# Optimization experiments

Measured on AMD Instinct MI355X. Metric: run time of the kernel, lower is better.

The kernel has to match this reference:

```python
import jax, jax.numpy as jnp
import numpy as np

B, T, C = 4, 1024, 2048
H, DN, DR = 16, 128, 64
D = DN + DR  # 192
Q_RANK, KV_RANK = 1536, 512
ROPE_BASE = 10000.0


def rope_cos_sin(seq_len, dim, dtype=jnp.float32):
    inv_freq = 1.0 / (ROPE_BASE ** (jnp.arange(0, dim, 2, dtype=jnp.float32) / dim))
    t = jnp.arange(seq_len, dtype=jnp.float32)
    freqs = jnp.outer(t, inv_freq)  # [T, dim/2]
    return jnp.cos(freqs).astype(dtype), jnp.sin(freqs).astype(dtype)


def apply_rope(x, cos, sin):
    # x: [B, T, H, Dr], cos/sin: [T, Dr/2]; interleaved-pair rotation (Llama style)
    x1 = x[..., 0::2]
    x2 = x[..., 1::2]
    c = cos[None, :, None, :]
    s = sin[None, :, None, :]
    o1 = x1 * c - x2 * s
    o2 = x1 * s + x2 * c
    return jnp.stack([o1, o2], axis=-1).reshape(x.shape)


def setup_inputs() -> dict:
    key = jax.random.key(0)
    ks = jax.random.split(key, 9)
    def g(k, shape, scale):
        return jax.random.normal(k, shape, dtype=jnp.float32) * scale
    return {
        "x": g(ks[0], (B, T, C), 1.0),
        "wq_down": g(ks[1], (C, Q_RANK), C ** -0.5),
        "wq_nope": g(ks[2], (Q_RANK, H * DN), Q_RANK ** -0.5),
        "wq_rope": g(ks[3], (Q_RANK, H * DR), Q_RANK ** -0.5),
        "wkv_down": g(ks[4], (C, KV_RANK), C ** -0.5),
        "wv_up": g(ks[5], (KV_RANK, H * D), KV_RANK ** -0.5),
        "wk_nope": g(ks[6], (KV_RANK, H * DN), KV_RANK ** -0.5),
        "wk_rope": g(ks[7], (KV_RANK, H * DR), KV_RANK ** -0.5),
        "wo": g(ks[8], (H * D, C), (H * D) ** -0.5),
    }


def reference(x, wq_down, wq_nope, wq_rope, wkv_down, wv_up, wk_nope, wk_rope, wo):
    b, t, c = x.shape
    q_latent = x @ wq_down            # [B,T,Q_RANK]
    kv_latent = x @ wkv_down          # [B,T,KV_RANK]
    q_c = (q_latent @ wq_nope).reshape(b, t, H, DN)
    q_r = (q_latent @ wq_rope).reshape(b, t, H, DR)
    v = (kv_latent @ wv_up).reshape(b, t, H, D)
    k_c = (kv_latent @ wk_nope).reshape(b, t, H, DN)
    k_r = (kv_latent @ wk_rope).reshape(b, t, H, DR)

    cos, sin = rope_cos_sin(t, DR, x.dtype)
    q_r = apply_rope(q_r, cos, sin)
    k_r = apply_rope(k_r, cos, sin)

    q = jnp.concatenate([q_c, q_r], axis=-1)  # [B,T,H,D]
    k = jnp.concatenate([k_c, k_r], axis=-1)  # [B,T,H,D]

    scale = 1.0 / (D ** 0.5)
    scores = jnp.einsum("bthd,bshd->bhts", q, k) * scale  # [B,H,T,T]
    causal = jnp.tril(jnp.ones((t, t), dtype=bool))
    scores = jnp.where(causal[None, None], scores, jnp.finfo(scores.dtype).min)
    probs = jax.nn.softmax(scores, axis=-1)
    out = jnp.einsum("bhts,bshd->bthd", probs, v).reshape(b, t, H * D)
    return out @ wo
```

## Files before the change

kernel.cpp:

```cpp
#include <hip/hip_runtime.h>

typedef unsigned short u16;
typedef __bf16  bf16x8 __attribute__((ext_vector_type(8)));
typedef short   short8 __attribute__((ext_vector_type(8)));
typedef float   f32x4  __attribute__((ext_vector_type(4)));
typedef u16     u16x4  __attribute__((ext_vector_type(4)));

__device__ __forceinline__ u16 f2bf(float f) {
  unsigned b = __builtin_bit_cast(unsigned, f);
  b += 0x7fffu + ((b >> 16) & 1u);
  return (u16)(b >> 16);
}
__device__ __forceinline__ float bf2f(u16 u) {
  return __builtin_bit_cast(float, (unsigned)u << 16);
}
__device__ __forceinline__ f32x4 mfma16(short8 a, short8 b, f32x4 c) {
  return __builtin_amdgcn_mfma_f32_16x16x32_bf16(
      __builtin_bit_cast(bf16x8, a), __builtin_bit_cast(bf16x8, b), c, 0, 0, 0);
}
__device__ __forceinline__ void gload_lds16(const void* g, void* l) {
  __builtin_amdgcn_global_load_lds(
      (const __attribute__((address_space(1))) void*)g,
      (__attribute__((address_space(3))) void*)l, 16, 0, 0);
}

#define VMCNT(n) asm volatile("s_waitcnt vmcnt(" #n ")" ::: "memory")
#define LGKMCNT(n) asm volatile("s_waitcnt lgkmcnt(" #n ")" ::: "memory")
#define MEMFENCE asm volatile("" ::: "memory")

__global__ __launch_bounds__(256) void castk(const float* __restrict__ in,
                                             u16* __restrict__ out, int n4) {
  int i = blockIdx.x * 256 + threadIdx.x;
  if (i >= n4) return;
  float4 v = ((const float4*)in)[i];
  u16x4 o;
  o[0] = f2bf(v.x); o[1] = f2bf(v.y); o[2] = f2bf(v.z); o[3] = f2bf(v.w);
  *(u16x4*)&out[i * 4] = o;
}

__global__ __launch_bounds__(256) void wcast(
    const float* __restrict__ wqd, const float* __restrict__ wqn,
    const float* __restrict__ wqr, const float* __restrict__ wkd,
    const float* __restrict__ wvu, const float* __restrict__ wkn,
    const float* __restrict__ wkr, const float* __restrict__ wo,
    u16* __restrict__ W1t, u16* __restrict__ Wqt,
    u16* __restrict__ Wkvt, u16* __restrict__ Wot) {
  __shared__ float tile[64][65];
  const int bid = blockIdx.x;
  const float* W; u16* Wt; int K, N, lid;
  if (bid < 768)       { W = wqd; Wt = W1t;                 K = 2048; N = 1536; lid = bid; }
  else if (bid < 1024) { W = wkd; Wt = W1t + 1536ull * 2048; K = 2048; N = 512;  lid = bid - 768; }
  else if (bid < 1792) { W = wqn; Wt = Wqt;                 K = 1536; N = 2048; lid = bid - 1024; }
  else if (bid < 2176) { W = wqr; Wt = Wqt + 2048ull * 1536; K = 1536; N = 1024; lid = bid - 1792; }
  else if (bid < 2432) { W = wkn; Wt = Wkvt;                K = 512;  N = 2048; lid = bid - 2176; }
  else if (bid < 2560) { W = wkr; Wt = Wkvt + 2048ull * 512; K = 512;  N = 1024; lid = bid - 2432; }
  else if (bid < 2944) { W = wvu; Wt = Wkvt + 3072ull * 512; K = 512;  N = 3072; lid = bid - 2560; }
  else                 { W = wo;  Wt = Wot;                 K = 3072; N = 2048; lid = bid - 2944; }
  const int kb = K >> 6;
  const int k0 = (lid % kb) * 64, n0 = (lid / kb) * 64;
  const int tid = threadIdx.x;
  const int lane4 = (tid & 15) * 4, grp = tid >> 4;
#pragma unroll
  for (int p = 0; p < 4; ++p) {
    int r = p * 16 + grp;
    float4 v = *(const float4*)&W[(size_t)(k0 + r) * N + n0 + lane4];
    tile[r][lane4]     = v.x;
    tile[r][lane4 + 1] = v.y;
    tile[r][lane4 + 2] = v.z;
    tile[r][lane4 + 3] = v.w;
  }
  __syncthreads();
  const int n = tid >> 2, ks = (tid & 3) * 16;
  short8 s0, s1;
#pragma unroll
  for (int j = 0; j < 8; ++j) s0[j] = (short)f2bf(tile[ks + j][n]);
#pragma unroll
  for (int j = 0; j < 8; ++j) s1[j] = (short)f2bf(tile[ks + 8 + j][n]);
  u16* dst = Wt + (size_t)(n0 + n) * K + k0 + ks;
  *(short8*)dst = s0;
  *(short8*)(dst + 8) = s1;
}

template <int EPI>
__global__ __launch_bounds__(512, 2) void gemm_p8(const u16* __restrict__ A, int lda,
                                                  const u16* __restrict__ Bt, int ldb,
                                                  void* __restrict__ out0,
                                                  void* __restrict__ out1,
                                                  void* __restrict__ out2, int ldc,
                                                  int K) {
  __shared__ char smem[147456];
  const int tid = threadIdx.x;
  const int w = tid >> 6, l = tid & 63;
  const int wr = w >> 2, wc = w & 3;
  const int lr = l & 15, hi = l >> 4, lg4 = hi * 4;

  const int nbx = gridDim.x;
  int id = blockIdx.y * nbx + blockIdx.x;
  int cpx = (nbx * gridDim.y) >> 3;
  int sid = (id & 7) * cpx + (id >> 3);
  const int m0 = (sid % nbx) * 128, n0 = (sid / nbx) * 256;

  const u16* asrc[2];
  const u16* bsrc[4];
#pragma unroll
  for (int j = 0; j < 2; ++j) {
    int lin = j * 8192 + tid * 16;
    int row = lin >> 7, colb = lin & 127;
    asrc[j] = A + (size_t)(m0 + row) * lda + ((colb ^ ((row & 7) << 4)) >> 1);
  }
#pragma unroll
  for (int j = 0; j < 4; ++j) {
    int lin = j * 8192 + tid * 16;
    int row = lin >> 7, colb = lin & 127;
    bsrc[j] = Bt + (size_t)(n0 + row) * ldb + ((colb ^ ((row & 7) << 4)) >> 1);
  }

  int aoff[4], boff[4];
#pragma unroll
  for (int m = 0; m < 4; ++m) {
    int row = wr * 64 + m * 16 + lr;
    aoff[m] = row * 128 + ((hi * 16) ^ ((row & 7) << 4));
  }
#pragma unroll
  for (int n = 0; n < 4; ++n) {
    int row = wc * 64 + n * 16 + lr;
    boff[n] = 16384 + row * 128 + ((hi * 16) ^ ((row & 7) << 4));
  }

  auto STAGE0 = [&](int kt) {
    char* buf = smem + 49152 * (kt % 3) + (w << 10);
    const int ke = kt << 6;
    gload_lds16(asrc[0] + ke, buf);
    gload_lds16(asrc[1] + ke, buf + 8192);
    gload_lds16(bsrc[0] + ke, buf + 16384);
    gload_lds16(bsrc[1] + ke, buf + 24576);
  };
  auto STAGE1 = [&](int kt) {
    char* buf = smem + 49152 * (kt % 3) + (w << 10);
    const int ke = kt << 6;
    gload_lds16(bsrc[2] + ke, buf + 32768);
    gload_lds16(bsrc[3] + ke, buf + 40960);
  };

  f32x4 acc[4][4] = {};
  const int NT = K >> 6;

  STAGE0(0); STAGE1(0); STAGE0(1); STAGE1(1);

  for (int kt = 0; kt < NT; ++kt) {
    if (kt < NT - 1) { VMCNT(6); } else { VMCNT(0); }
    __builtin_amdgcn_s_barrier();
    MEMFENCE;
    const char* buf = smem + 49152 * (kt % 3);
    {
      short8 a0[4], b0[4];
#pragma unroll
      for (int m = 0; m < 4; ++m) a0[m] = *(const short8*)(buf + aoff[m]);
#pragma unroll
      for (int n = 0; n < 4; ++n) b0[n] = *(const short8*)(buf + boff[n]);
      if (kt + 2 < NT) STAGE0(kt + 2);
      LGKMCNT(0);
      __builtin_amdgcn_sched_barrier(0);
      __builtin_amdgcn_s_setprio(1);
#pragma unroll
      for (int m = 0; m < 4; ++m)
#pragma unroll
        for (int n = 0; n < 4; ++n) acc[m][n] = mfma16(a0[m], b0[n], acc[m][n]);
      __builtin_amdgcn_s_setprio(0);
    }
    MEMFENCE;
    __builtin_amdgcn_s_barrier();
    MEMFENCE;
    {
      short8 a1[4], b1[4];
#pragma unroll
      for (int m = 0; m < 4; ++m) a1[m] = *(const short8*)(buf + (aoff[m] ^ 64));
#pragma unroll
      for (int n = 0; n < 4; ++n) b1[n] = *(const short8*)(buf + (boff[n] ^ 64));
      if (kt + 2 < NT) STAGE1(kt + 2);
      LGKMCNT(0);
      __builtin_amdgcn_sched_barrier(0);
      __builtin_amdgcn_s_setprio(1);
#pragma unroll
      for (int m = 0; m < 4; ++m)
#pragma unroll
        for (int n = 0; n < 4; ++n) acc[m][n] = mfma16(a1[m], b1[n], acc[m][n]);
      __builtin_amdgcn_s_setprio(0);
    }
    MEMFENCE;
  }

  if (EPI == 3 && n0 >= 3072) {
    __syncthreads();
    u16* ldt = (u16*)smem;
#pragma unroll
    for (int m = 0; m < 4; ++m)
#pragma unroll
      for (int n = 0; n < 4; ++n)
#pragma unroll
        for (int j = 0; j < 4; ++j)
          ldt[(wc * 64 + n * 16 + lr) * 136 + (wr * 64 + m * 16 + lg4 + j)] =
              f2bf(acc[m][n][j]);
    __syncthreads();
    const int b = m0 >> 10, tloc = m0 & 1023, n0v = n0 - 3072;
#pragma unroll
    for (int i = 0; i < 8; ++i) {
      int lin = i * 512 + tid;
      int col = lin >> 4, t16 = lin & 15;
      int cg = n0v + col;
      int h = (unsigned)cg / 192u, d = cg - h * 192;
      short8 vv = *(const short8*)&ldt[col * 136 + t16 * 8];
      *(short8*)((u16*)out2 + ((size_t)(b * 16 + h) * 192 + d) * 1024 + tloc + t16 * 8) = vv;
    }
    return;
  }
#pragma unroll
  for (int m = 0; m < 4; ++m)
#pragma unroll
    for (int n = 0; n < 4; ++n)
#pragma unroll
      for (int j = 0; j < 4; ++j) {
        int r = m0 + wr * 64 + m * 16 + lg4 + j;
        int c = n0 + wc * 64 + n * 16 + lr;
        float v = acc[m][n][j];
        if (EPI == 0) {
          ((u16*)out0)[(size_t)r * ldc + c] = f2bf(v);
        } else if (EPI == 1 || EPI == 3) {
          if (c < 2048) {
            int cc = (c >> 7) * 192 + (c & 127);
            ((u16*)out0)[(size_t)r * ldc + cc] = f2bf(v);
          } else {
            ((u16*)out1)[(size_t)r * 1024 + (c - 2048)] = f2bf(v);
          }
        } else {
          ((float*)out0)[(size_t)r * ldc + c] = v;
        }
      }
}

__global__ __launch_bounds__(256) void rope_k(const u16* __restrict__ qsrc,
                                              const u16* __restrict__ ksrc,
                                              u16* __restrict__ qdst,
                                              u16* __restrict__ kdst) {
  int idx = blockIdx.x * 256 + threadIdx.x;
  int row = idx >> 9;
  int rem = idx & 511;
  int h = rem >> 5, i = rem & 31;
  int tpos = row & 1023;
  float inv = exp2f(-(float)i * 0.4152410118609203f);
  float f = (float)tpos * inv;
  float s, c;
  sincosf(f, &s, &c);
  size_t si = (size_t)row * 1024 + h * 64 + 2 * i;
  size_t o = (size_t)row * 3072 + h * 192 + 128 + 2 * i;
  {
    float x1 = bf2f(qsrc[si]), x2 = bf2f(qsrc[si + 1]);
    qdst[o]     = f2bf(x1 * c - x2 * s);
    qdst[o + 1] = f2bf(x1 * s + x2 * c);
  }
  {
    float x1 = bf2f(ksrc[si]), x2 = bf2f(ksrc[si + 1]);
    kdst[o]     = f2bf(x1 * c - x2 * s);
    kdst[o + 1] = f2bf(x1 * s + x2 * c);
  }
}

__global__ __launch_bounds__(256, 2) void attn_kernel(const u16* __restrict__ Q,
                                                      const u16* __restrict__ K,
                                                      const u16* __restrict__ Vt,
                                                      u16* __restrict__ O) {
  __shared__ char smem[57344];
  const int t = threadIdx.x, w = t >> 6, l = t & 63;
  const int lr = l & 15, hi = l >> 4;
  const int y = blockIdx.y;
  const int qidx = (y < 4) ? 2 * y : 15 - 2 * y;
  const int qb = qidx * 128;
  const int bh = blockIdx.x;
  const int b = bh >> 4, h = bh & 15;
  const int wq0 = qb + w * 32;
  const size_t rs = 3072;
  const u16* Qg = Q + ((size_t)(b * 1024 + qb)) * rs + h * 192;
  const char* Kg = (const char*)(K + ((size_t)b * 1024) * rs + h * 192);
  const char* Vg = (const char*)(Vt + (size_t)(b * 16 + h) * 192 * 1024);
  u16* Og = O + ((size_t)(b * 1024 + qb)) * rs + h * 192;

  char* psw = smem + 49152 + w * 2048;
  const int kswz = (lr & 7) << 4;
  const int pswz = (lr & 3) << 4;

  short8 qfr[2][6];
#pragma unroll
  for (int qf = 0; qf < 2; ++qf)
#pragma unroll
    for (int dc = 0; dc < 6; ++dc)
      qfr[qf][dc] = *(const short8*)(Qg + (size_t)(w * 32 + qf * 16 + lr) * rs + dc * 32 + hi * 8);

  const char* kptr[3];
#pragma unroll
  for (int i = 0; i < 3; ++i) {
    int lin = (i * 4 + w) * 1024 + l * 16;
    int row = lin / 384;
    int col = lin % 384;
    kptr[i] = Kg + (size_t)row * 6144 + (col ^ ((row & 7) << 4));
  }
  const char* vptr[3];
#pragma unroll
  for (int i = 0; i < 3; ++i) {
    int lin = (i * 4 + w) * 1024 + l * 16;
    int row = lin >> 6;
    int col = lin & 63;
    vptr[i] = Vg + (size_t)row * 2048 + (col ^ ((row & 3) << 4));
  }

  f32x4 o[12][2] = {};
  float m[2] = {-1e30f, -1e30f}, ls[2] = {0.f, 0.f};
  const float scale = 0.07216878364870323f;
  const int nkv = 4 * (qidx + 1);

  auto STAGE = [&](int kt) {
    char* kb = smem + (kt & 1) * 24576;
    char* vb = kb + 12288;
#pragma unroll
    for (int i = 0; i < 3; ++i) {
      gload_lds16(kptr[i] + (size_t)kt * 196608, kb + (i * 4 + w) * 1024);
      gload_lds16(vptr[i] + (size_t)kt * 64,     vb + (i * 4 + w) * 1024);
    }
  };

  STAGE(0);
  for (int kt = 0; kt < nkv; ++kt) {
    if (kt + 1 < nkv) { STAGE(kt + 1); VMCNT(6); }
    else              { VMCNT(0); }
    __builtin_amdgcn_s_barrier();
    MEMFENCE;
    const int kv0 = kt << 5;
    const char* ks = smem + (kt & 1) * 24576;
    const char* vs = ks + 12288;

    if (kv0 <= wq0) {
      f32x4 st[2][2] = {};
#pragma unroll
      for (int dc = 0; dc < 6; ++dc) {
        const int kin = (dc * 64 + hi * 16) ^ kswz;
        short8 ka0 = *(const short8*)(ks + lr * 384 + kin);
        short8 ka1 = *(const short8*)(ks + (16 + lr) * 384 + kin);
        st[0][0] = mfma16(ka0, qfr[0][dc], st[0][0]);
        st[0][1] = mfma16(ka0, qfr[1][dc], st[0][1]);
        st[1][0] = mfma16(ka1, qfr[0][dc], st[1][0]);
        st[1][1] = mfma16(ka1, qfr[1][dc], st[1][1]);
      }

      const bool needmask = (kv0 + 31 > wq0);
      float mt[2];
#pragma unroll
      for (int qf = 0; qf < 2; ++qf) {
        const int q = wq0 + qf * 16 + lr;
        float mx = -1e30f;
#pragma unroll
        for (int kf = 0; kf < 2; ++kf)
#pragma unroll
          for (int j = 0; j < 4; ++j) {
            float s = st[kf][qf][j] * scale;
            if (needmask && (kv0 + kf * 16 + hi * 4 + j > q)) s = -1e30f;
            st[kf][qf][j] = s;
            mx = fmaxf(mx, s);
          }
        mx = fmaxf(mx, __shfl_xor(mx, 16));
        mx = fmaxf(mx, __shfl_xor(mx, 32));
        mt[qf] = mx;
      }
      const bool skip = __all((mt[0] <= m[0] + 8.0f) & (mt[1] <= m[1] + 8.0f));
      if (!skip) {
#pragma unroll
        for (int qf = 0; qf < 2; ++qf) {
          float mn = fmaxf(m[qf], mt[qf]);
          float corr = __expf(m[qf] - mn);
          m[qf] = mn;
          ls[qf] *= corr;
#pragma unroll
          for (int nf = 0; nf < 12; ++nf)
#pragma unroll
            for (int j = 0; j < 4; ++j) o[nf][qf][j] *= corr;
        }
      }
#pragma unroll
      for (int qf = 0; qf < 2; ++qf) {
        float sum = 0.f;
        char* pq = psw + (qf * 16 + lr) * 64;
#pragma unroll
        for (int kf = 0; kf < 2; ++kf)
#pragma unroll
          for (int jp = 0; jp < 2; ++jp) {
            float p0 = __expf(st[kf][qf][2 * jp]     - m[qf]);
            float p1 = __expf(st[kf][qf][2 * jp + 1] - m[qf]);
            sum += p0 + p1;
            unsigned pk = (unsigned)f2bf(p0) | ((unsigned)f2bf(p1) << 16);
            int kb = 2 * (kf * 16 + hi * 4 + 2 * jp);
            *(unsigned*)(pq + (kb ^ pswz)) = pk;
          }
        sum += __shfl_xor(sum, 16);
        sum += __shfl_xor(sum, 32);
        ls[qf] += sum;
      }
      asm volatile("s_waitcnt lgkmcnt(0)" ::: "memory");
      __builtin_amdgcn_sched_barrier(0);

      short8 pb0 = *(const short8*)(psw + lr * 64 + ((hi * 16) ^ pswz));
      short8 pb1 = *(const short8*)(psw + (16 + lr) * 64 + ((hi * 16) ^ pswz));
#pragma unroll
      for (int nf = 0; nf < 12; ++nf) {
        short8 va = *(const short8*)(vs + (nf * 16 + lr) * 64 + ((hi * 16) ^ pswz));
        o[nf][0] = mfma16(va, pb0, o[nf][0]);
        o[nf][1] = mfma16(va, pb1, o[nf][1]);
      }
    }
    MEMFENCE;
    __builtin_amdgcn_s_barrier();
  }

#pragma unroll
  for (int qf = 0; qf < 2; ++qf) {
    float inv = 1.0f / ls[qf];
    char* ob = smem + (w * 32 + qf * 16 + lr) * 384;
#pragma unroll
    for (int nf = 0; nf < 12; ++nf)
#pragma unroll
      for (int j = 0; j < 4; ++j)
        *(u16*)(ob + ((nf * 32 + hi * 8 + 2 * j) ^ kswz)) = f2bf(o[nf][qf][j] * inv);
  }
  __syncthreads();
#pragma unroll
  for (int i = 0; i < 12; ++i) {
    int idx = i * 256 + t;
    int row = idx / 24;
    int c16 = idx % 24;
    short8 vv = *(const short8*)(smem + row * 384 + ((c16 * 16) ^ ((row & 7) << 4)));
    *(short8*)((char*)Og + (size_t)row * 6144 + c16 * 16) = vv;
  }
}

extern "C" void kernel_launch(void* const* d_in, const int* in_sizes, int n_in,
                              void* d_out, int out_size, void* d_ws, size_t ws_size,
                              hipStream_t stream) {
  const float* x   = (const float*)d_in[0];
  const float* wqd = (const float*)d_in[1];
  const float* wqn = (const float*)d_in[2];
  const float* wqr = (const float*)d_in[3];
  const float* wkd = (const float*)d_in[4];
  const float* wvu = (const float*)d_in[5];
  const float* wkn = (const float*)d_in[6];
  const float* wkr = (const float*)d_in[7];
  const float* wo  = (const float*)d_in[8];

  char* ws = (char*)d_ws;
  size_t off = 0;
  auto alloc = [&](size_t bytes) {
    char* p = ws + off;
    off += (bytes + 255) & ~(size_t)255;
    return p;
  };
  u16* xb   = (u16*)alloc(8388608ull * 2);
  u16* W1t  = (u16*)alloc(2048ull * 2048 * 2);
  u16* Wqt  = (u16*)alloc(3072ull * 1536 * 2);
  u16* Wkvt = (u16*)alloc(6144ull * 512 * 2);
  u16* Wot  = (u16*)alloc(2048ull * 3072 * 2);
  u16* lat  = (u16*)alloc(4096ull * 2048 * 2);
  u16* Qb   = (u16*)alloc(4096ull * 3072 * 2);
  u16* Kb   = (u16*)alloc(4096ull * 3072 * 2);
  u16* Vt   = (u16*)alloc(4096ull * 3072 * 2);
  u16* AO   = (u16*)alloc(4096ull * 3072 * 2);
  u16* qrt  = (u16*)alloc(4096ull * 1024 * 2);
  u16* krt  = (u16*)alloc(4096ull * 1024 * 2);

  castk<<<8192, 256, 0, stream>>>(x, xb, 2097152);

  wcast<<<4480, 256, 0, stream>>>(wqd, wqn, wqr, wkd, wvu, wkn, wkr, wo,
                                  W1t, Wqt, Wkvt, Wot);

  gemm_p8<0><<<dim3(32, 8), 512, 0, stream>>>(xb, 2048, W1t, 2048, lat, nullptr, nullptr, 2048, 2048);
  gemm_p8<1><<<dim3(32, 12), 512, 0, stream>>>(lat, 2048, Wqt, 1536, Qb, qrt, nullptr, 3072, 1536);
  gemm_p8<3><<<dim3(32, 24), 512, 0, stream>>>(lat + 1536, 2048, Wkvt, 512, Kb, krt, Vt, 3072, 512);

  rope_k<<<8192, 256, 0, stream>>>(qrt, krt, Qb, Kb);

  attn_kernel<<<dim3(64, 8), 256, 0, stream>>>(Qb, Kb, Vt, AO);

  gemm_p8<2><<<dim3(32, 8), 512, 0, stream>>>(AO, 3072, Wot, 3072, d_out, nullptr, nullptr, 2048, 3072);
}
```

Baseline: 270.5 us.

## Pair complementary 64-row query tiles per block for causal load balance

```diff
diff --git a/kernel.cpp b/kernel.cpp
--- a/kernel.cpp
+++ b/kernel.cpp
@@ -1,4 +1,5 @@
 #include <hip/hip_runtime.h>
+#include <type_traits>
 
 typedef unsigned short u16;
 typedef __bf16  bf16x8 __attribute__((ext_vector_type(8)));
@@ -269,31 +270,28 @@
                                                       const u16* __restrict__ K,
                                                       const u16* __restrict__ Vt,
                                                       u16* __restrict__ O) {
-  __shared__ char smem[57344];
+  __shared__ char smem[53248];
   const int t = threadIdx.x, w = t >> 6, l = t & 63;
   const int lr = l & 15, hi = l >> 4;
   const int y = blockIdx.y;
-  const int qidx = (y < 4) ? 2 * y : 15 - 2 * y;
-  const int qb = qidx * 128;
   const int bh = blockIdx.x;
   const int b = bh >> 4, h = bh & 15;
-  const int wq0 = qb + w * 32;
   const size_t rs = 3072;
-  const u16* Qg = Q + ((size_t)(b * 1024 + qb)) * rs + h * 192;
+  const int tb[2] = { y * 64, (15 - y) * 64 };
   const char* Kg = (const char*)(K + ((size_t)b * 1024) * rs + h * 192);
   const char* Vg = (const char*)(Vt + (size_t)(b * 16 + h) * 192 * 1024);
-  u16* Og = O + ((size_t)(b * 1024 + qb)) * rs + h * 192;
-
-  char* psw = smem + 49152 + w * 2048;
+
+  char* psw = smem + 49152 + w * 1024;
   const int kswz = (lr & 7) << 4;
   const int pswz = (lr & 3) << 4;
 
   short8 qfr[2][6];
 #pragma unroll
-  for (int qf = 0; qf < 2; ++qf)
+  for (int g = 0; g < 2; ++g)
 #pragma unroll
     for (int dc = 0; dc < 6; ++dc)
-      qfr[qf][dc] = *(const short8*)(Qg + (size_t)(w * 32 + qf * 16 + lr) * rs + dc * 32 + hi * 8);
+      qfr[g][dc] = *(const short8*)(Q + (size_t)(b * 1024 + tb[g] + w * 16 + lr) * rs
+                                    + h * 192 + dc * 32 + hi * 8);
 
   const char* kptr[3];
 #pragma unroll
@@ -315,84 +313,78 @@
   f32x4 o[12][2] = {};
   float m[2] = {-1e30f, -1e30f}, ls[2] = {0.f, 0.f};
   const float scale = 0.07216878364870323f;
-  const int nkv = 4 * (qidx + 1);
-
-  auto STAGE = [&](int kt) {
-    char* kb = smem + (kt & 1) * 24576;
+  const int nkv1 = 2 * (y + 1);
+  const int NIT = 34;
+
+  auto STAGE = [&](int it) {
+    const int kvt = (it < nkv1) ? it : it - nkv1;
+    char* kb = smem + (it & 1) * 24576;
     char* vb = kb + 12288;
 #pragma unroll
     for (int i = 0; i < 3; ++i) {
-      gload_lds16(kptr[i] + (size_t)kt * 196608, kb + (i * 4 + w) * 1024);
-      gload_lds16(vptr[i] + (size_t)kt * 64,     vb + (i * 4 + w) * 1024);
+      gload_lds16(kptr[i] + (size_t)kvt * 196608, kb + (i * 4 + w) * 1024);
+      gload_lds16(vptr[i] + (size_t)kvt * 64,     vb + (i * 4 + w) * 1024);
     }
   };
 
   STAGE(0);
-  for (int kt = 0; kt < nkv; ++kt) {
-    if (kt + 1 < nkv) { STAGE(kt + 1); VMCNT(6); }
+  for (int it = 0; it < NIT; ++it) {
+    if (it + 1 < NIT) { STAGE(it + 1); VMCNT(6); }
     else              { VMCNT(0); }
     __builtin_amdgcn_s_barrier();
     MEMFENCE;
-    const int kv0 = kt << 5;
-    const char* ks = smem + (kt & 1) * 24576;
+    const int kvt = (it < nkv1) ? it : it - nkv1;
+    const int kv0 = kvt << 5;
+    const char* ks = smem + (it & 1) * 24576;
     const char* vs = ks + 12288;
 
-    if (kv0 <= wq0) {
-      f32x4 st[2][2] = {};
+    auto body = [&](auto GTAG) {
+      constexpr int g = decltype(GTAG)::value;
+      const int wq0 = tb[g] + w * 16;
+      if (kv0 > wq0 + 15) return;
+      f32x4 st[2] = {};
 #pragma unroll
       for (int dc = 0; dc < 6; ++dc) {
         const int kin = (dc * 64 + hi * 16) ^ kswz;
         short8 ka0 = *(const short8*)(ks + lr * 384 + kin);
         short8 ka1 = *(const short8*)(ks + (16 + lr) * 384 + kin);
-        st[0][0] = mfma16(ka0, qfr[0][dc], st[0][0]);
-        st[0][1] = mfma16(ka0, qfr[1][dc], st[0][1]);
-        st[1][0] = mfma16(ka1, qfr[0][dc], st[1][0]);
-        st[1][1] = mfma16(ka1, qfr[1][dc], st[1][1]);
+        st[0] = mfma16(ka0, qfr[g][dc], st[0]);
+        st[1] = mfma16(ka1, qfr[g][dc], st[1]);
       }
-
       const bool needmask = (kv0 + 31 > wq0);
-      float mt[2];
-#pragma unroll
-      for (int qf = 0; qf < 2; ++qf) {
-        const int q = wq0 + qf * 16 + lr;
-        float mx = -1e30f;
+      const int q = wq0 + lr;
+      float mx = -1e30f;
+#pragma unroll
+      for (int kf = 0; kf < 2; ++kf)
+#pragma unroll
+        for (int j = 0; j < 4; ++j) {
+          float s = st[kf][j] * scale;
+          if (needmask && (kv0 + kf * 16 + hi * 4 + j > q)) s = -1e30f;
+          st[kf][j] = s;
+          mx = fmaxf(mx, s);
+        }
+      mx = fmaxf(mx, __shfl_xor(mx, 16));
+      mx = fmaxf(mx, __shfl_xor(mx, 32));
+      const bool skip = __all(mx <= m[g] + 8.0f);
+      if (!skip) {
+        float mn = fmaxf(m[g], mx);
+        float corr = __expf(m[g] - mn);
+        m[g] = mn;
+        ls[g] *= corr;
+#pragma unroll
+        for (int nf = 0; nf < 12; ++nf)
+#pragma unroll
+          for (int j = 0; j < 4; ++j) o[nf][g][j] *= corr;
+      }
+      {
+        float sum = 0.f;
+        char* pq = psw + lr * 64;
 #pragma unroll
         for (int kf = 0; kf < 2; ++kf)
 #pragma unroll
-          for (int j = 0; j < 4; ++j) {
-            float s = st[kf][qf][j] * scale;
-            if (needmask && (kv0 + kf * 16 + hi * 4 + j > q)) s = -1e30f;
-            st[kf][qf][j] = s;
-            mx = fmaxf(mx, s);
-          }
-        mx = fmaxf(mx, __shfl_xor(mx, 16));
-        mx = fmaxf(mx, __shfl_xor(mx, 32));
-        mt[qf] = mx;
-      }
-      const bool skip = __all((mt[0] <= m[0] + 8.0f) & (mt[1] <= m[1] + 8.0f));
-      if (!skip) {
-#pragma unroll
-        for (int qf = 0; qf < 2; ++qf) {
-          float mn = fmaxf(m[qf], mt[qf]);
-          float corr = __expf(m[qf] - mn);
-          m[qf] = mn;
-          ls[qf] *= corr;
-#pragma unroll
-          for (int nf = 0; nf < 12; ++nf)
-#pragma unroll
-            for (int j = 0; j < 4; ++j) o[nf][qf][j] *= corr;
-        }
-      }
-#pragma unroll
-      for (int qf = 0; qf < 2; ++qf) {
-        float sum = 0.f;
-        char* pq = psw + (qf * 16 + lr) * 64;
-#pragma unroll
-        for (int kf = 0; kf < 2; ++kf)
-#pragma unroll
           for (int jp = 0; jp < 2; ++jp) {
-            float p0 = __expf(st[kf][qf][2 * jp]     - m[qf]);
-            float p1 = __expf(st[kf][qf][2 * jp + 1] - m[qf]);
+            float p0 = __expf(st[kf][2 * jp]     - m[g]);
+            float p1 = __expf(st[kf][2 * jp + 1] - m[g]);
             sum += p0 + p1;
             unsigned pk = (unsigned)f2bf(p0) | ((unsigned)f2bf(p1) << 16);
             int kb = 2 * (kf * 16 + hi * 4 + 2 * jp);
@@ -400,43 +392,48 @@
           }
         sum += __shfl_xor(sum, 16);
         sum += __shfl_xor(sum, 32);
-        ls[qf] += sum;
+        ls[g] += sum;
       }
       asm volatile("s_waitcnt lgkmcnt(0)" ::: "memory");
       __builtin_amdgcn_sched_barrier(0);
-
-      short8 pb0 = *(const short8*)(psw + lr * 64 + ((hi * 16) ^ pswz));
-      short8 pb1 = *(const short8*)(psw + (16 + lr) * 64 + ((hi * 16) ^ pswz));
+      short8 pb = *(const short8*)(psw + lr * 64 + ((hi * 16) ^ pswz));
 #pragma unroll
       for (int nf = 0; nf < 12; ++nf) {
         short8 va = *(const short8*)(vs + (nf * 16 + lr) * 64 + ((hi * 16) ^ pswz));
-        o[nf][0] = mfma16(va, pb0, o[nf][0]);
-        o[nf][1] = mfma16(va, pb1, o[nf][1]);
+        o[nf][g] = mfma16(va, pb, o[nf][g]);
       }
-    }
+    };
+    if (it < nkv1) body(std::integral_constant<int, 0>{});
+    else           body(std::integral_constant<int, 1>{});
+
     MEMFENCE;
     __builtin_amdgcn_s_barrier();
   }
 
 #pragma unroll
-  for (int qf = 0; qf < 2; ++qf) {
-    float inv = 1.0f / ls[qf];
-    char* ob = smem + (w * 32 + qf * 16 + lr) * 384;
+  for (int g = 0; g < 2; ++g) {
+    float inv = 1.0f / ls[g];
+    char* ob = smem + (g * 64 + w * 16 + lr) * 384;
 #pragma unroll
     for (int nf = 0; nf < 12; ++nf)
 #pragma unroll
       for (int j = 0; j < 4; ++j)
-        *(u16*)(ob + ((nf * 32 + hi * 8 + 2 * j) ^ kswz)) = f2bf(o[nf][qf][j] * inv);
+        *(u16*)(ob + ((nf * 32 + hi * 8 + 2 * j) ^ kswz)) = f2bf(o[nf][g][j] * inv);
   }
   __syncthreads();
+  const u16* dummy;
+  u16* Og0 = O + ((size_t)(b * 1024 + tb[0])) * rs + h * 192;
+  u16* Og1 = O + ((size_t)(b * 1024 + tb[1])) * rs + h * 192;
 #pragma unroll
   for (int i = 0; i < 12; ++i) {
     int idx = i * 256 + t;
     int row = idx / 24;
     int c16 = idx % 24;
     short8 vv = *(const short8*)(smem + row * 384 + ((c16 * 16) ^ ((row & 7) << 4)));
-    *(short8*)((char*)Og + (size_t)row * 6144 + c16 * 16) = vv;
-  }
+    u16* base = (row < 64) ? (Og0 + (size_t)row * rs) : (Og1 + (size_t)(row - 64) * rs);
+    *(short8*)((char*)base + c16 * 16) = vv;
+  }
+  (void)dummy;
 }
 
 extern "C" void kernel_launch(void* const* d_in, const int* in_sizes, int n_in,
```

New measurement: 276.2 us. 1.02x slower.
